# Kernel optimization log

Measured on AMD Instinct MI355X. Metric: run time of the kernel, lower is better.

## Reference

```python
import math
import jax, jax.numpy as jnp
import numpy as np

NUM_LAYERS = 2
D = 128
H = 8
CTX = 16
B, M, T = 4, 16, 256


def _lin(x, W, b):
    # torch nn.Linear: y = x @ W^T + b, W: [out, in]
    return jnp.einsum('...d,ed->...e', x, W) + b


def _ln(x, g, b, eps=1e-6):
    mu = jnp.mean(x, axis=-1, keepdims=True)
    v = jnp.mean((x - mu) ** 2, axis=-1, keepdims=True)
    return (x - mu) / jnp.sqrt(v + eps) * g + b


def _context_attention(x, L):
    # Faithful vectorization of the per-position python loop in ContextAttention.
    # Zero left-padding is NOT masked in the softmax (pad keys give score 0),
    # exactly as in the torch original.
    b, m, t, d = x.shape
    xp = jnp.pad(x, ((0, 0), (0, 0), (L - 1, 0), (0, 0)))  # [b,m,t+L-1,d]
    idx = jnp.arange(t)[:, None] + jnp.arange(L)[None, :]   # [t,L] window indices
    win = xp[:, :, idx, :]                                  # [b,m,t,L,d]
    scores = jnp.einsum('bmtd,bmtld->bmtl', x, win) / math.sqrt(d)
    w = jax.nn.softmax(scores, axis=-1)
    return jnp.einsum('bmtl,bmtld->bmtd', w, win)


def setup_inputs():
    key = jax.random.key(0)
    ks = jax.random.split(key, 8)
    L = NUM_LAYERS

    def w(k, shape):
        return jax.random.normal(k, shape, dtype=jnp.float32) * 0.02

    return {
        'x': jax.random.normal(ks[0], (B, M, T, D), dtype=jnp.float32),
        'Wq': w(ks[1], (L, D, D)), 'bq': jnp.zeros((L, D), jnp.float32),
        'Wk': w(ks[2], (L, D, D)), 'bk': jnp.zeros((L, D), jnp.float32),
        'Wv': w(ks[3], (L, D, D)), 'bv': jnp.zeros((L, D), jnp.float32),
        'Wo': w(ks[4], (L, D, D)), 'bo': jnp.zeros((L, D), jnp.float32),
        'W1': w(ks[5], (L, 4 * D, D)), 'b1': jnp.zeros((L, 4 * D), jnp.float32),
        'W2': w(ks[6], (L, D, 4 * D)), 'b2': jnp.zeros((L, D), jnp.float32),
        'ln1_g': jnp.ones((L, D), jnp.float32), 'ln1_b': jnp.zeros((L, D), jnp.float32),
        'ln2_g': jnp.ones((L, D), jnp.float32), 'ln2_b': jnp.zeros((L, D), jnp.float32),
        'lnf_g': jnp.ones((D,), jnp.float32), 'lnf_b': jnp.zeros((D,), jnp.float32),
        'context_len': CTX,
    }


def reference(x, Wq, bq, Wk, bk, Wv, bv, Wo, bo, W1, b1, W2, b2,
              ln1_g, ln1_b, ln2_g, ln2_b, lnf_g, lnf_b, context_len):
    b, m, t, d = x.shape
    dk = d // H

    def mha(xin, i):
        q = _lin(xin, Wq[i], bq[i])
        k = _lin(xin, Wk[i], bk[i])
        v = _lin(xin, Wv[i], bv[i])
        cq = _context_attention(q, context_len).reshape(b, m, t, H, dk)
        ck = _context_attention(k, context_len).reshape(b, m, t, H, dk)
        vr = v.reshape(b, m, t, H, dk)
        # full attention over time axis
        s = jnp.einsum('bmqhd,bmkhd->bmhqk', cq, ck) / math.sqrt(dk)
        xa = jnp.einsum('bmhqk,bmkhd->bmqhd', jax.nn.softmax(s, axis=-1), vr)
        # relational attention over the asset axis m
        s2 = jnp.einsum('bqthd,bkthd->bthqk', xa, xa) / math.sqrt(dk)
        xr = jnp.einsum('bthqk,bkthd->bthqd', jax.nn.softmax(s2, axis=-1), xa)
        # torch: permute((3,0,1,2,4)) -> [m,b,t,h,dk], then .view(b,m,t,d)
        xr = jnp.transpose(xr, (3, 0, 1, 2, 4)).reshape(b, m, t, d)
        return _lin(xr, Wo[i], bo[i])

    def ffn(xin, i):
        return _lin(jax.nn.relu(_lin(xin, W1[i], b1[i])), W2[i], b2[i])

    y = x
    for i in range(Wq.shape[0]):
        y = y + mha(_ln(y, ln1_g[i], ln1_b[i]), i)
        y = y + ffn(_ln(y, ln2_g[i], ln2_b[i]), i)
    return _ln(y, lnf_g, lnf_b)
```

## Files before the change

### kernel.cpp

```cpp
#include <hip/hip_runtime.h>
#include <cstddef>
#include <cstdint>

static constexpr int D_ = 128;
static constexpr int NROW = 16384;
static constexpr size_t S_ = (size_t)NROW * D_;

typedef __attribute__((ext_vector_type(8))) short bf16x8;
typedef __attribute__((ext_vector_type(4))) float f32x4;
typedef __attribute__((ext_vector_type(16))) float f32x16;
typedef __attribute__((ext_vector_type(8))) unsigned short ushortx8;

__device__ __forceinline__ unsigned short f2bf(float f) {
  unsigned int u = __float_as_uint(f);
  u += 0x7fff + ((u >> 16) & 1);
  return (unsigned short)(u >> 16);
}
__device__ __forceinline__ float bf2f(unsigned short h) {
  return __uint_as_float(((unsigned int)h) << 16);
}
__device__ __forceinline__ unsigned int cvt_pk_bf16(float lo, float hi) {
  unsigned int r;
  asm volatile("v_cvt_pk_bf16_f32 %0, %1, %2" : "=v"(r) : "v"(lo), "v"(hi));
  return r;
}
__device__ __forceinline__ float wsum64(float s) {
#pragma unroll
  for (int off = 32; off >= 1; off >>= 1) s += __shfl_xor(s, off);
  return s;
}

__global__ __launch_bounds__(256) void prep_kernel(
    const float* __restrict__ X,
    const float* __restrict__ Wq, const float* __restrict__ Wk,
    const float* __restrict__ Wv, const float* __restrict__ Wo,
    const float* __restrict__ W1, const float* __restrict__ W2,
    const float* __restrict__ bq, const float* __restrict__ bk,
    const float* __restrict__ bv, const float* __restrict__ bo,
    const float* __restrict__ b1, const float* __restrict__ b2,
    const float* __restrict__ g, const float* __restrict__ b,
    unsigned short* __restrict__ Wb, float* __restrict__ Bs,
    unsigned short* __restrict__ Ab) {
  int bx = blockIdx.x;
  if (bx < 192) {
    size_t i = ((size_t)bx * 256 + threadIdx.x) * 8;
    int layer = i >= 196608;
    size_t o = i - (size_t)layer * 196608;
    const float* src; size_t off;
    if      (o < 16384)  { src = Wq + layer * 16384; off = o; }
    else if (o < 32768)  { src = Wk + layer * 16384; off = o - 16384; }
    else if (o < 49152)  { src = Wv + layer * 16384; off = o - 32768; }
    else if (o < 65536)  { src = Wo + layer * 16384; off = o - 49152; }
    else if (o < 131072) { src = W1 + layer * 65536; off = o - 65536; }
    else                 { src = W2 + layer * 65536; off = o - 131072; }
    ushortx8 r;
#pragma unroll
    for (int j = 0; j < 8; j++) r[j] = f2bf(src[off + j]);
    *(ushortx8*)(Wb + i) = r;
  } else if (bx < 201) {
    int tid = (bx - 192) * 256 + threadIdx.x;
    if (tid >= 2304) return;
    int layer = tid / 1152, o = tid % 1152;
    float v;
    if      (o < 128)  v = bq[layer * 128 + o];
    else if (o < 256)  v = bk[layer * 128 + o - 128];
    else if (o < 384)  v = bv[layer * 128 + o - 256];
    else if (o < 512)  v = bo[layer * 128 + o - 384];
    else if (o < 1024) v = b1[layer * 512 + o - 512];
    else               v = b2[layer * 128 + o - 1024];
    Bs[tid] = v;
  } else {
    int wid = threadIdx.x >> 6, lane = threadIdx.x & 63;
    int row = ((bx - 201) << 2) + wid;
    float2 xv = *(const float2*)(X + (size_t)row * D_ + lane * 2);
    float s = wsum64(xv.x + xv.y);
    float sq = wsum64(xv.x * xv.x + xv.y * xv.y);
    float mu = s * (1.0f / 128.0f);
    float var = sq * (1.0f / 128.0f) - mu * mu;
    float rstd = rsqrtf(var + 1e-6f);
    float2 gv = *(const float2*)(g + lane * 2);
    float2 bv2 = *(const float2*)(b + lane * 2);
    unsigned int lo = f2bf((xv.x - mu) * rstd * gv.x + bv2.x);
    unsigned int hi = f2bf((xv.y - mu) * rstd * gv.y + bv2.y);
    *(unsigned int*)(Ab + (size_t)row * D_ + lane * 2) = lo | (hi << 16);
  }
}

template <int NT, int ROWW>
__global__ __launch_bounds__(512, 2) void gemm_kernel(
    const unsigned short* __restrict__ A, int lda,
    const unsigned short* __restrict__ W, int ldw,
    const float* __restrict__ bias,
    unsigned short* __restrict__ Cb, int K) {
  constexpr int COLW = 8 / ROWW;
  const int w = threadIdx.x >> 6;
  const int l = threadIdx.x & 63;
  const int rw = w / COLW, cw = w % COLW;
  const int r0 = blockIdx.x * (16 * ROWW) + rw * 16;
  const int c0 = cw * (NT * 16);
  const int lr = l & 15, lk = (l >> 4) * 8;
  f32x4 acc[NT] = {};
  const unsigned short* Ap = A + (size_t)(r0 + lr) * lda + lk;
  const unsigned short* Wp = W + (size_t)(c0 + lr) * ldw + lk;
  for (int kb = 0; kb < K; kb += 128) {
    bf16x8 aF[4];
    bf16x8 wF[4][NT];
#pragma unroll
    for (int kt = 0; kt < 4; ++kt) {
      int k0 = kb + kt * 32;
      aF[kt] = *(const bf16x8*)(Ap + k0);
#pragma unroll
      for (int n = 0; n < NT; ++n)
        wF[kt][n] = *(const bf16x8*)(Wp + (size_t)(n * 16) * ldw + k0);
    }
#pragma unroll
    for (int kt = 0; kt < 4; ++kt)
#pragma unroll
      for (int n = 0; n < NT; ++n)
        acc[n] = __builtin_amdgcn_mfma_f32_16x16x32_bf16(aF[kt], wF[kt][n], acc[n], 0, 0, 0);
  }
  const int rb = (l >> 4) * 4;
#pragma unroll
  for (int n = 0; n < NT; ++n) {
    int col = c0 + n * 16 + lr;
    float bval = bias[col];
    unsigned short* dst = Cb + (size_t)(col >> 7) * S_ + (col & 127);
#pragma unroll
    for (int j = 0; j < 4; ++j)
      dst[(size_t)(r0 + rb + j) * 128] = f2bf(acc[n][j] + bval);
  }
}

static constexpr int LDH = 136;
__global__ __launch_bounds__(512, 2) void ffn_kernel(
    const unsigned short* __restrict__ Abuf,
    const unsigned short* __restrict__ Wo_, const unsigned short* __restrict__ W1_,
    const unsigned short* __restrict__ W2_, const float* __restrict__ Bl,
    const float* __restrict__ rin,
    const float* __restrict__ ln2G, const float* __restrict__ ln2B,
    const float* __restrict__ lnxG, const float* __restrict__ lnxB,
    float* __restrict__ Yout, unsigned short* __restrict__ AbOut, int finalMode) {
  __shared__ unsigned short As[64][LDH];
  __shared__ unsigned short Hs[64][LDH];
  __shared__ unsigned short Mid[64][LDH];
  __shared__ float2 lnred[64][8];
  const int tid = threadIdx.x;
  const int w = tid >> 6, l = tid & 63;
  const int r0 = blockIdx.x * 64;
  const int lr = l & 15, lk = (l >> 4) * 8, rb = (l >> 4) * 4;
  const int col = w * 16 + lr;

  bf16x8 wof[4], w1f[4], w2f[4];
#pragma unroll
  for (int kt = 0; kt < 4; ++kt) {
    wof[kt] = *(const bf16x8*)(Wo_ + (size_t)col * 128 + kt * 32 + lk);
    w1f[kt] = *(const bf16x8*)(W1_ + (size_t)col * 128 + kt * 32 + lk);
    w2f[kt] = *(const bf16x8*)(W2_ + (size_t)col * 512 + kt * 32 + lk);
  }
#pragma unroll
  for (int itr = 0; itr < 2; ++itr) {
    int idx = itr * 512 + tid;
    int r = idx >> 4, c8 = (idx & 15) * 8;
    *(ushortx8*)&As[r][c8] = *(const ushortx8*)(Abuf + (size_t)(r0 + r) * 128 + c8);
  }
  __syncthreads();

  f32x4 acc1[4] = {};
#pragma unroll
  for (int kt = 0; kt < 4; ++kt)
#pragma unroll
    for (int m = 0; m < 4; ++m) {
      bf16x8 a = *(const bf16x8*)&As[m * 16 + lr][kt * 32 + lk];
      acc1[m] = __builtin_amdgcn_mfma_f32_16x16x32_bf16(a, wof[kt], acc1[m], 0, 0, 0);
    }
  float yreg[4][4];
  {
    float bval = Bl[384 + col];
#pragma unroll
    for (int m = 0; m < 4; ++m)
#pragma unroll
      for (int j = 0; j < 4; ++j)
        yreg[m][j] = acc1[m][j] + bval + rin[(size_t)(r0 + m * 16 + rb + j) * 128 + col];
  }
  {
    float s[4][4], sq[4][4];
#pragma unroll
    for (int m = 0; m < 4; ++m)
#pragma unroll
      for (int j = 0; j < 4; ++j) { s[m][j] = yreg[m][j]; sq[m][j] = yreg[m][j] * yreg[m][j]; }
#pragma unroll
    for (int off = 1; off < 16; off <<= 1)
#pragma unroll
      for (int m = 0; m < 4; ++m)
#pragma unroll
        for (int j = 0; j < 4; ++j) {
          s[m][j] += __shfl_xor(s[m][j], off);
          sq[m][j] += __shfl_xor(sq[m][j], off);
        }
    if (lr == 0)
#pragma unroll
      for (int m = 0; m < 4; ++m)
#pragma unroll
        for (int j = 0; j < 4; ++j)
          lnred[m * 16 + rb + j][w] = make_float2(s[m][j], sq[m][j]);
    __syncthreads();
    if (tid < 64) {
      float ts = 0.f, tq = 0.f;
#pragma unroll
      for (int k = 0; k < 8; ++k) { float2 p = lnred[tid][k]; ts += p.x; tq += p.y; }
      float mu = ts * (1.0f / 128.0f);
      float rstd = rsqrtf(tq * (1.0f / 128.0f) - mu * mu + 1e-6f);
      lnred[tid][0] = make_float2(mu, rstd);
    }
    __syncthreads();
    float g = ln2G[col], bb = ln2B[col];
#pragma unroll
    for (int m = 0; m < 4; ++m)
#pragma unroll
      for (int j = 0; j < 4; ++j) {
        float2 st = lnred[m * 16 + rb + j][0];
        Hs[m * 16 + rb + j][col] = f2bf((yreg[m][j] - st.x) * st.y * g + bb);
      }
  }
  __syncthreads();
  f32x4 acc2[4] = {};
#pragma unroll
  for (int c = 0; c < 4; ++c) {
    bf16x8 w1n[4], w2n[4];
    if (c < 3) {
#pragma unroll
      for (int kt = 0; kt < 4; ++kt) {
        w1n[kt] = *(const bf16x8*)(W1_ + (size_t)((c + 1) * 128 + col) * 128 + kt * 32 + lk);
        w2n[kt] = *(const bf16x8*)(W2_ + (size_t)col * 512 + (c + 1) * 128 + kt * 32 + lk);
      }
    }
    f32x4 accm[4] = {};
#pragma unroll
    for (int kt = 0; kt < 4; ++kt)
#pragma unroll
      for (int m = 0; m < 4; ++m) {
        bf16x8 a = *(const bf16x8*)&Hs[m * 16 + lr][kt * 32 + lk];
        accm[m] = __builtin_amdgcn_mfma_f32_16x16x32_bf16(a, w1f[kt], accm[m], 0, 0, 0);
      }
    float b1v = Bl[512 + c * 128 + col];
#pragma unroll
    for (int m = 0; m < 4; ++m)
#pragma unroll
      for (int j = 0; j < 4; ++j)
        Mid[m * 16 + rb + j][col] = f2bf(fmaxf(accm[m][j] + b1v, 0.f));
    __syncthreads();
#pragma unroll
    for (int kt = 0; kt < 4; ++kt)
#pragma unroll
      for (int m = 0; m < 4; ++m) {
        bf16x8 a = *(const bf16x8*)&Mid[m * 16 + lr][kt * 32 + lk];
        acc2[m] = __builtin_amdgcn_mfma_f32_16x16x32_bf16(a, w2f[kt], acc2[m], 0, 0, 0);
      }
    __syncthreads();
    if (c < 3) {
#pragma unroll
      for (int kt = 0; kt < 4; ++kt) { w1f[kt] = w1n[kt]; w2f[kt] = w2n[kt]; }
    }
  }
  float vfin[4][4];
  {
    float bval = Bl[1024 + col];
    float s[4][4], sq[4][4];
#pragma unroll
    for (int m = 0; m < 4; ++m)
#pragma unroll
      for (int j = 0; j < 4; ++j) {
        float v = acc2[m][j] + bval + yreg[m][j];
        vfin[m][j] = v;
        s[m][j] = v;
        sq[m][j] = v * v;
      }
#pragma unroll
    for (int off = 1; off < 16; off <<= 1)
#pragma unroll
      for (int m = 0; m < 4; ++m)
#pragma unroll
        for (int j = 0; j < 4; ++j) {
          s[m][j] += __shfl_xor(s[m][j], off);
          sq[m][j] += __shfl_xor(sq[m][j], off);
        }
    if (lr == 0)
#pragma unroll
      for (int m = 0; m < 4; ++m)
#pragma unroll
        for (int j = 0; j < 4; ++j)
          lnred[m * 16 + rb + j][w] = make_float2(s[m][j], sq[m][j]);
    __syncthreads();
    if (tid < 64) {
      float ts = 0.f, tq = 0.f;
#pragma unroll
      for (int k = 0; k < 8; ++k) { float2 p = lnred[tid][k]; ts += p.x; tq += p.y; }
      float mu = ts * (1.0f / 128.0f);
      float rstd = rsqrtf(tq * (1.0f / 128.0f) - mu * mu + 1e-6f);
      lnred[tid][0] = make_float2(mu, rstd);
    }
    __syncthreads();
    float g = lnxG[col], bb = lnxB[col];
#pragma unroll
    for (int m = 0; m < 4; ++m)
#pragma unroll
      for (int j = 0; j < 4; ++j) {
        int row = r0 + m * 16 + rb + j;
        float2 st = lnred[m * 16 + rb + j][0];
        float t = (vfin[m][j] - st.x) * st.y * g + bb;
        if (finalMode == 0) {
          Yout[(size_t)row * 128 + col] = vfin[m][j];
          AbOut[(size_t)row * 128 + col] = f2bf(t);
        } else {
          Yout[(size_t)row * 128 + col] = t;
        }
      }
  }
}

static constexpr int CTXLD = 134;
__global__ __launch_bounds__(128) void ctx_kernel(
    const unsigned short* __restrict__ qin, const unsigned short* __restrict__ kin,
    unsigned short* __restrict__ cqo, unsigned short* __restrict__ cko) {
  __shared__ float xs[47 * CTXLD];
  const unsigned short* src = blockIdx.y ? kin : qin;
  unsigned short* dst = blockIdx.y ? cko : cqo;
  const size_t rbase = (size_t)blockIdx.x * 256;
  const int t0 = blockIdx.z * 32;
  const int tid = threadIdx.x;
#pragma unroll
  for (int it = 0; it < 6; ++it) {
    int idx = it * 128 + tid;
    int i = idx >> 4, c8 = (idx & 15) * 8;
    if (i < 47) {
      int rg = t0 - 15 + i;
      float f[8];
      if (rg >= 0) {
        ushortx8 wv = *(const ushortx8*)(src + (rbase + rg) * 128 + c8);
#pragma unroll
        for (int j = 0; j < 8; ++j) f[j] = bf2f(wv[j]);
      } else {
#pragma unroll
        for (int j = 0; j < 8; ++j) f[j] = 0.f;
      }
      int base = i * CTXLD + c8 + (c8 >> 5) * 2;
#pragma unroll
      for (int j = 0; j < 8; j += 2)
        *(float2*)&xs[base + j] = make_float2(f[j], f[j + 1]);
    }
  }
  __syncthreads();
  const int ql = tid >> 2, qu = tid & 3;
  const int cb = qu * 34;
  const int cg = qu * 32;
  float ow[32];
#pragma unroll
  for (int c = 0; c < 32; c += 2) {
    float2 w = *(const float2*)&xs[(ql + 15) * CTXLD + cb + c];
    ow[c] = w.x; ow[c + 1] = w.y;
  }
  float p[16];
#pragma unroll
  for (int l = 0; l < 16; ++l) {
    const float* row = &xs[(ql + l) * CTXLD + cb];
    float d = 0.f;
#pragma unroll
    for (int c = 0; c < 32; c += 2) {
      float2 w = *(const float2*)(row + c);
      d = fmaf(ow[c], w.x, d);
      d = fmaf(ow[c + 1], w.y, d);
    }
    p[l] = d;
  }
  float den = 0.f;
#pragma unroll
  for (int l = 0; l < 16; ++l) {
    float sc = p[l] + __shfl_xor(p[l], 1);
    sc += __shfl_xor(sc, 2);
    p[l] = __expf(sc * 0.08838834764831845f);
    den += p[l];
  }
  float o[32];
#pragma unroll
  for (int c = 0; c < 32; ++c) o[c] = 0.f;
#pragma unroll
  for (int l = 0; l < 16; ++l) {
    float pl = p[l];
    const float* row = &xs[(ql + l) * CTXLD + cb];
#pragma unroll
    for (int c = 0; c < 32; c += 2) {
      float2 w = *(const float2*)(row + c);
      o[c] = fmaf(pl, w.x, o[c]);
      o[c + 1] = fmaf(pl, w.y, o[c + 1]);
    }
  }
  float inv = 1.0f / den;
  unsigned short* op = dst + (rbase + t0 + ql) * 128 + cg;
#pragma unroll
  for (int c8 = 0; c8 < 4; ++c8) {
    ushortx8 r;
#pragma unroll
    for (int j = 0; j < 8; ++j) r[j] = f2bf(o[c8 * 8 + j] * inv);
    *(ushortx8*)(op + c8 * 8) = r;
  }
}

static constexpr int PW = 272;
__global__ __launch_bounds__(256) void attn1_kernel(
    const unsigned short* __restrict__ cq, const unsigned short* __restrict__ ck,
    unsigned short* __restrict__ v) {
  __shared__ unsigned short vt[16][PW];
  __shared__ unsigned short ps[4][32][PW];
  __shared__ float rsum[4][32];
  const int bm = blockIdx.x >> 3, h = blockIdx.x & 7;
  const size_t rbase = (size_t)bm * 256;
  const int cbase = h * 16;
  const int tid = threadIdx.x;
  {
    ushortx8 v0 = *(const ushortx8*)(v + (rbase + tid) * 128 + cbase);
    ushortx8 v1 = *(const ushortx8*)(v + (rbase + tid) * 128 + cbase + 8);
#pragma unroll
    for (int d = 0; d < 8; ++d) { vt[d][tid] = v0[d]; vt[8 + d][tid] = v1[d]; }
  }
  __syncthreads();
  const int wid = tid >> 6, lane = tid & 63;
  const int l31 = lane & 31, l15 = lane & 15;
  const int hi5 = lane >> 5, hi4 = lane >> 4;
#pragma unroll
  for (int qt = 0; qt < 2; ++qt) {
    const int q0 = (wid * 2 + qt) * 32;
    bf16x8 bq = *(const bf16x8*)(cq + (rbase + q0 + l31) * 128 + cbase + hi5 * 8);
    float lsum = 0.f;
#pragma unroll
    for (int kt = 0; kt < 8; ++kt) {
      bf16x8 ak = *(const bf16x8*)(ck + (rbase + kt * 32 + l31) * 128 + cbase + hi5 * 8);
      f32x16 z = {};
      f32x16 s = __builtin_amdgcn_mfma_f32_32x32x16_bf16(ak, bq, z, 0, 0, 0);
      float p[16];
#pragma unroll
      for (int r = 0; r < 16; ++r) { p[r] = __expf(s[r] * 0.25f); lsum += p[r]; }
#pragma unroll
      for (int r = 0; r < 16; r += 2) {
        unsigned int pk = cvt_pk_bf16(p[r], p[r + 1]);
        int key = kt * 32 + (r & 3) + 8 * (r >> 2) + 4 * hi5;
        *(unsigned int*)&ps[wid][l31][key] = pk;
      }
    }
    lsum += __shfl_xor(lsum, 32);
    if (lane < 32) rsum[wid][lane] = 1.0f / lsum;
#pragma unroll
    for (int m = 0; m < 2; ++m) {
      f32x4 o = {};
#pragma unroll
      for (int k2 = 0; k2 < 8; ++k2) {
        bf16x8 pa = *(const bf16x8*)&ps[wid][m * 16 + l15][k2 * 32 + hi4 * 8];
        bf16x8 vb = *(const bf16x8*)&vt[l15][k2 * 32 + hi4 * 8];
        o = __builtin_amdgcn_mfma_f32_16x16x32_bf16(pa, vb, o, 0, 0, 0);
      }
      unsigned short* dst = v + (rbase + q0 + m * 16 + hi4 * 4) * 128 + cbase + l15;
#pragma unroll
      for (int j = 0; j < 4; ++j) {
        float inv = rsum[wid][m * 16 + hi4 * 4 + j];
        dst[(size_t)j * 128] = f2bf(o[j] * inv);
      }
    }
  }
}

__global__ __launch_bounds__(128) void attn2_kernel(
    const unsigned short* __restrict__ xa, unsigned short* __restrict__ xr) {
  __shared__ float xas[16][128];
  int b = blockIdx.x >> 8, t = blockIdx.x & 255;
  int tid = threadIdx.x;
#pragma unroll
  for (int jj = 0; jj < 2; ++jj) {
    int idx = tid + (jj << 7);
    int r = idx >> 4, c8 = (idx & 15) * 8;
    ushortx8 vv = *(const ushortx8*)(xa + ((size_t)((b * 16 + r) * 256 + t)) * 128 + c8);
#pragma unroll
    for (int j = 0; j < 8; ++j) xas[r][c8 + j] = bf2f(vv[j]);
  }
  __syncthreads();
  int h = tid >> 4, q = tid & 15;
  float xq[16];
#pragma unroll
  for (int d = 0; d < 16; d++) xq[d] = xas[q][h * 16 + d];
  float sc[16];
  float mx = -1e30f;
#pragma unroll
  for (int k = 0; k < 16; k++) {
    float s = 0.f;
#pragma unroll
    for (int d = 0; d < 16; d++) s += xq[d] * xas[k][h * 16 + d];
    s *= 0.25f;
    sc[k] = s;
    mx = fmaxf(mx, s);
  }
  float den = 0.f;
#pragma unroll
  for (int k = 0; k < 16; k++) { sc[k] = __expf(sc[k] - mx); den += sc[k]; }
  float inv = 1.0f / den;
  float out[16] = {};
#pragma unroll
  for (int k = 0; k < 16; k++) {
    float w = sc[k];
#pragma unroll
    for (int d = 0; d < 16; d++) out[d] += w * xas[k][h * 16 + d];
  }
  int g = q * 4 + b;
  unsigned short* dstp = xr + ((size_t)(g * 256 + t)) * 128 + h * 16;
  ushortx8 r0;
#pragma unroll
  for (int j = 0; j < 8; ++j) r0[j] = f2bf(out[j] * inv);
  *(ushortx8*)dstp = r0;
#pragma unroll
  for (int j = 0; j < 8; ++j) r0[j] = f2bf(out[8 + j] * inv);
  *(ushortx8*)(dstp + 8) = r0;
}

extern "C" void kernel_launch(void* const* d_in, const int* in_sizes, int n_in,
                              void* d_out, int out_size, void* d_ws, size_t ws_size,
                              hipStream_t stream) {
  const float* x    = (const float*)d_in[0];
  const float* Wq   = (const float*)d_in[1];
  const float* bq   = (const float*)d_in[2];
  const float* Wk   = (const float*)d_in[3];
  const float* bk   = (const float*)d_in[4];
  const float* Wv   = (const float*)d_in[5];
  const float* bv   = (const float*)d_in[6];
  const float* Wo   = (const float*)d_in[7];
  const float* bo   = (const float*)d_in[8];
  const float* W1   = (const float*)d_in[9];
  const float* b1   = (const float*)d_in[10];
  const float* W2   = (const float*)d_in[11];
  const float* b2   = (const float*)d_in[12];
  const float* ln1g = (const float*)d_in[13];
  const float* ln1b = (const float*)d_in[14];
  const float* ln2g = (const float*)d_in[15];
  const float* ln2b = (const float*)d_in[16];
  const float* lnfg = (const float*)d_in[17];
  const float* lnfb = (const float*)d_in[18];

  char* base = (char*)d_ws;
  unsigned short* CQb = (unsigned short*)base;
  unsigned short* CKb = (unsigned short*)(base + (4u  << 20));
  unsigned short* Qb  = (unsigned short*)(base + (8u  << 20));
  unsigned short* Kb  = (unsigned short*)(base + (12u << 20));
  unsigned short* Vb  = (unsigned short*)(base + (16u << 20));
  unsigned short* Ab  = (unsigned short*)(base + (20u << 20));
  unsigned short* Wb  = (unsigned short*)(base + (24u << 20));
  float*          Bs  = (float*)(base + (24u << 20) + 786432);
  float*          Y   = (float*)d_out;

  prep_kernel<<<4297, 256, 0, stream>>>(x, Wq, Wk, Wv, Wo, W1, W2,
                                        bq, bk, bv, bo, b1, b2,
                                        ln1g, ln1b, Wb, Bs, Ab);

  for (int i = 0; i < 2; ++i) {
    const float* rin = i ? Y : x;
    const unsigned short* Wl = Wb + (size_t)i * 196608;
    const float* Bl = Bs + i * 1152;
    gemm_kernel<3, 1><<<1024, 512, 0, stream>>>(Ab, 128, Wl, 128, Bl, Qb, 128);
    ctx_kernel<<<dim3(64, 2, 8), 128, 0, stream>>>(Qb, Kb, CQb, CKb);
    attn1_kernel<<<512, 256, 0, stream>>>(CQb, CKb, Vb);
    attn2_kernel<<<1024, 128, 0, stream>>>(Vb, Ab);
    if (i == 0) {
      ffn_kernel<<<256, 512, 0, stream>>>(Ab, Wl + 49152, Wl + 65536, Wl + 131072, Bl,
          rin, ln2g, ln2b, ln1g + 128, ln1b + 128, Y, Ab, 0);
    } else {
      ffn_kernel<<<256, 512, 0, stream>>>(Ab, Wl + 49152, Wl + 65536, Wl + 131072, Bl,
          rin, ln2g + 128, ln2b + 128, lnfg, lnfb, Y, nullptr, 1);
    }
  }
}
```

Measured before the change: 186.9 us.

## Retile FFN kernel to 32-row blocks with 4 waves covering 32 columns each

The fused Wo+LN+FFN kernel now processes 32 rows per block with 256 threads, and each wave computes two 16-column tiles instead of one. This doubles the grid from 256 to 512 blocks, which fills more of the CUs, and lets each A-fragment read from shared memory feed two MFMAs. It also removes one barrier per layernorm by having every lane reduce the per-row statistics itself, and it loads the residual input early. In exchange, each wave holds more registers for weight fragments, and weights are re-read by twice as many blocks.

```diff
diff --git a/kernel.cpp b/kernel.cpp
--- a/kernel.cpp
+++ b/kernel.cpp
@@ -132,7 +132,7 @@
 }
 
 static constexpr int LDH = 136;
-__global__ __launch_bounds__(512, 2) void ffn_kernel(
+__global__ __launch_bounds__(256, 2) void ffn_kernel(
     const unsigned short* __restrict__ Abuf,
     const unsigned short* __restrict__ Wo_, const unsigned short* __restrict__ W1_,
     const unsigned short* __restrict__ W2_, const float* __restrict__ Bl,
@@ -140,58 +140,77 @@
     const float* __restrict__ ln2G, const float* __restrict__ ln2B,
     const float* __restrict__ lnxG, const float* __restrict__ lnxB,
     float* __restrict__ Yout, unsigned short* __restrict__ AbOut, int finalMode) {
-  __shared__ unsigned short As[64][LDH];
-  __shared__ unsigned short Hs[64][LDH];
-  __shared__ unsigned short Mid[64][LDH];
-  __shared__ float2 lnred[64][8];
+  __shared__ unsigned short As[32][LDH];
+  __shared__ unsigned short Hs[32][LDH];
+  __shared__ unsigned short Mid[32][LDH];
+  __shared__ float2 lnred[32][4];
   const int tid = threadIdx.x;
   const int w = tid >> 6, l = tid & 63;
-  const int r0 = blockIdx.x * 64;
+  const int r0 = blockIdx.x * 32;
   const int lr = l & 15, lk = (l >> 4) * 8, rb = (l >> 4) * 4;
-  const int col = w * 16 + lr;
-
-  bf16x8 wof[4], w1f[4], w2f[4];
-#pragma unroll
-  for (int kt = 0; kt < 4; ++kt) {
-    wof[kt] = *(const bf16x8*)(Wo_ + (size_t)col * 128 + kt * 32 + lk);
-    w1f[kt] = *(const bf16x8*)(W1_ + (size_t)col * 128 + kt * 32 + lk);
-    w2f[kt] = *(const bf16x8*)(W2_ + (size_t)col * 512 + kt * 32 + lk);
+  const int cbase = w * 32;
+
+  float rv[2][2][4];
+#pragma unroll
+  for (int m = 0; m < 2; ++m)
+#pragma unroll
+    for (int n = 0; n < 2; ++n) {
+      int col = cbase + n * 16 + lr;
+#pragma unroll
+      for (int j = 0; j < 4; ++j)
+        rv[m][n][j] = rin[(size_t)(r0 + m * 16 + rb + j) * 128 + col];
+    }
+  bf16x8 wof[4][2], w1f[4][2];
+#pragma unroll
+  for (int n = 0; n < 2; ++n) {
+    int col = cbase + n * 16 + lr;
+#pragma unroll
+    for (int kt = 0; kt < 4; ++kt) {
+      wof[kt][n] = *(const bf16x8*)(Wo_ + (size_t)col * 128 + kt * 32 + lk);
+      w1f[kt][n] = *(const bf16x8*)(W1_ + (size_t)col * 128 + kt * 32 + lk);
+    }
   }
 #pragma unroll
   for (int itr = 0; itr < 2; ++itr) {
-    int idx = itr * 512 + tid;
+    int idx = itr * 256 + tid;
     int r = idx >> 4, c8 = (idx & 15) * 8;
     *(ushortx8*)&As[r][c8] = *(const ushortx8*)(Abuf + (size_t)(r0 + r) * 128 + c8);
   }
   __syncthreads();
 
-  f32x4 acc1[4] = {};
+  f32x4 acc1[2][2] = {};
 #pragma unroll
   for (int kt = 0; kt < 4; ++kt)
 #pragma unroll
-    for (int m = 0; m < 4; ++m) {
+    for (int m = 0; m < 2; ++m) {
       bf16x8 a = *(const bf16x8*)&As[m * 16 + lr][kt * 32 + lk];
-      acc1[m] = __builtin_amdgcn_mfma_f32_16x16x32_bf16(a, wof[kt], acc1[m], 0, 0, 0);
-    }
-  float yreg[4][4];
+#pragma unroll
+      for (int n = 0; n < 2; ++n)
+        acc1[m][n] = __builtin_amdgcn_mfma_f32_16x16x32_bf16(a, wof[kt][n], acc1[m][n], 0, 0, 0);
+    }
+  float yreg[2][2][4];
+#pragma unroll
+  for (int n = 0; n < 2; ++n) {
+    float bval = Bl[384 + cbase + n * 16 + lr];
+#pragma unroll
+    for (int m = 0; m < 2; ++m)
+#pragma unroll
+      for (int j = 0; j < 4; ++j)
+        yreg[m][n][j] = acc1[m][n][j] + bval + rv[m][n][j];
+  }
   {
-    float bval = Bl[384 + col];
-#pragma unroll
-    for (int m = 0; m < 4; ++m)
-#pragma unroll
-      for (int j = 0; j < 4; ++j)
-        yreg[m][j] = acc1[m][j] + bval + rin[(size_t)(r0 + m * 16 + rb + j) * 128 + col];
-  }
-  {
-    float s[4][4], sq[4][4];
-#pragma unroll
-    for (int m = 0; m < 4; ++m)
-#pragma unroll
-      for (int j = 0; j < 4; ++j) { s[m][j] = yreg[m][j]; sq[m][j] = yreg[m][j] * yreg[m][j]; }
+    float s[2][4], sq[2][4];
+#pragma unroll
+    for (int m = 0; m < 2; ++m)
+#pragma unroll
+      for (int j = 0; j < 4; ++j) {
+        s[m][j] = yreg[m][0][j] + yreg[m][1][j];
+        sq[m][j] = yreg[m][0][j] * yreg[m][0][j] + yreg[m][1][j] * yreg[m][1][j];
+      }
 #pragma unroll
     for (int off = 1; off < 16; off <<= 1)
 #pragma unroll
-      for (int m = 0; m < 4; ++m)
+      for (int m = 0; m < 2; ++m)
 #pragma unroll
         for (int j = 0; j < 4; ++j) {
           s[m][j] += __shfl_xor(s[m][j], off);
@@ -199,86 +218,105 @@
         }
     if (lr == 0)
 #pragma unroll
-      for (int m = 0; m < 4; ++m)
+      for (int m = 0; m < 2; ++m)
 #pragma unroll
         for (int j = 0; j < 4; ++j)
           lnred[m * 16 + rb + j][w] = make_float2(s[m][j], sq[m][j]);
     __syncthreads();
-    if (tid < 64) {
-      float ts = 0.f, tq = 0.f;
-#pragma unroll
-      for (int k = 0; k < 8; ++k) { float2 p = lnred[tid][k]; ts += p.x; tq += p.y; }
-      float mu = ts * (1.0f / 128.0f);
-      float rstd = rsqrtf(tq * (1.0f / 128.0f) - mu * mu + 1e-6f);
-      lnred[tid][0] = make_float2(mu, rstd);
+#pragma unroll
+    for (int m = 0; m < 2; ++m)
+#pragma unroll
+      for (int j = 0; j < 4; ++j) {
+        int row = m * 16 + rb + j;
+        float ts = 0.f, tq = 0.f;
+#pragma unroll
+        for (int k = 0; k < 4; ++k) { float2 p = lnred[row][k]; ts += p.x; tq += p.y; }
+        float mu = ts * (1.0f / 128.0f);
+        float rstd = rsqrtf(tq * (1.0f / 128.0f) - mu * mu + 1e-6f);
+#pragma unroll
+        for (int n = 0; n < 2; ++n) {
+          int col = cbase + n * 16 + lr;
+          Hs[row][col] = f2bf((yreg[m][n][j] - mu) * rstd * ln2G[col] + ln2B[col]);
+        }
+      }
+  }
+  __syncthreads();
+  f32x4 acc2[2][2] = {};
+#pragma unroll
+  for (int c = 0; c < 4; ++c) {
+    bf16x8 w2f[4][2], w1n[4][2];
+#pragma unroll
+    for (int n = 0; n < 2; ++n) {
+      int col = cbase + n * 16 + lr;
+#pragma unroll
+      for (int kt = 0; kt < 4; ++kt) {
+        w2f[kt][n] = *(const bf16x8*)(W2_ + (size_t)col * 512 + c * 128 + kt * 32 + lk);
+        if (c < 3)
+          w1n[kt][n] = *(const bf16x8*)(W1_ + (size_t)((c + 1) * 128 + col) * 128 + kt * 32 + lk);
+      }
+    }
+    f32x4 accm[2][2] = {};
+#pragma unroll
+    for (int kt = 0; kt < 4; ++kt)
+#pragma unroll
+      for (int m = 0; m < 2; ++m) {
+        bf16x8 a = *(const bf16x8*)&Hs[m * 16 + lr][kt * 32 + lk];
+#pragma unroll
+        for (int n = 0; n < 2; ++n)
+          accm[m][n] = __builtin_amdgcn_mfma_f32_16x16x32_bf16(a, w1f[kt][n], accm[m][n], 0, 0, 0);
+      }
+#pragma unroll
+    for (int n = 0; n < 2; ++n) {
+      float b1v = Bl[512 + c * 128 + cbase + n * 16 + lr];
+      int col = cbase + n * 16 + lr;
+#pragma unroll
+      for (int m = 0; m < 2; ++m)
+#pragma unroll
+        for (int j = 0; j < 4; ++j)
+          Mid[m * 16 + rb + j][col] = f2bf(fmaxf(accm[m][n][j] + b1v, 0.f));
     }
     __syncthreads();
-    float g = ln2G[col], bb = ln2B[col];
-#pragma unroll
-    for (int m = 0; m < 4; ++m)
-#pragma unroll
-      for (int j = 0; j < 4; ++j) {
-        float2 st = lnred[m * 16 + rb + j][0];
-        Hs[m * 16 + rb + j][col] = f2bf((yreg[m][j] - st.x) * st.y * g + bb);
-      }
-  }
-  __syncthreads();
-  f32x4 acc2[4] = {};
-#pragma unroll
-  for (int c = 0; c < 4; ++c) {
-    bf16x8 w1n[4], w2n[4];
-    if (c < 3) {
-#pragma unroll
-      for (int kt = 0; kt < 4; ++kt) {
-        w1n[kt] = *(const bf16x8*)(W1_ + (size_t)((c + 1) * 128 + col) * 128 + kt * 32 + lk);
-        w2n[kt] = *(const bf16x8*)(W2_ + (size_t)col * 512 + (c + 1) * 128 + kt * 32 + lk);
-      }
-    }
-    f32x4 accm[4] = {};
 #pragma unroll
     for (int kt = 0; kt < 4; ++kt)
 #pragma unroll
-      for (int m = 0; m < 4; ++m) {
-        bf16x8 a = *(const bf16x8*)&Hs[m * 16 + lr][kt * 32 + lk];
-        accm[m] = __builtin_amdgcn_mfma_f32_16x16x32_bf16(a, w1f[kt], accm[m], 0, 0, 0);
-      }
-    float b1v = Bl[512 + c * 128 + col];
-#pragma unroll
-    for (int m = 0; m < 4; ++m)
-#pragma unroll
-      for (int j = 0; j < 4; ++j)
-        Mid[m * 16 + rb + j][col] = f2bf(fmaxf(accm[m][j] + b1v, 0.f));
-    __syncthreads();
-#pragma unroll
-    for (int kt = 0; kt < 4; ++kt)
-#pragma unroll
-      for (int m = 0; m < 4; ++m) {
+      for (int m = 0; m < 2; ++m) {
         bf16x8 a = *(const bf16x8*)&Mid[m * 16 + lr][kt * 32 + lk];
-        acc2[m] = __builtin_amdgcn_mfma_f32_16x16x32_bf16(a, w2f[kt], acc2[m], 0, 0, 0);
+#pragma unroll
+        for (int n = 0; n < 2; ++n)
+          acc2[m][n] = __builtin_amdgcn_mfma_f32_16x16x32_bf16(a, w2f[kt][n], acc2[m][n], 0, 0, 0);
       }
     __syncthreads();
     if (c < 3) {
 #pragma unroll
-      for (int kt = 0; kt < 4; ++kt) { w1f[kt] = w1n[kt]; w2f[kt] = w2n[kt]; }
-    }
-  }
-  float vfin[4][4];
+      for (int kt = 0; kt < 4; ++kt)
+#pragma unroll
+        for (int n = 0; n < 2; ++n) w1f[kt][n] = w1n[kt][n];
+    }
+  }
   {
-    float bval = Bl[1024 + col];
-    float s[4][4], sq[4][4];
-#pragma unroll
-    for (int m = 0; m < 4; ++m)
-#pragma unroll
-      for (int j = 0; j < 4; ++j) {
-        float v = acc2[m][j] + bval + yreg[m][j];
-        vfin[m][j] = v;
-        s[m][j] = v;
-        sq[m][j] = v * v;
-      }
+    float vfin[2][2][4];
+    float s[2][4], sq[2][4];
+#pragma unroll
+    for (int m = 0; m < 2; ++m)
+#pragma unroll
+      for (int j = 0; j < 4; ++j) { s[m][j] = 0.f; sq[m][j] = 0.f; }
+#pragma unroll
+    for (int n = 0; n < 2; ++n) {
+      float bval = Bl[1024 + cbase + n * 16 + lr];
+#pragma unroll
+      for (int m = 0; m < 2; ++m)
+#pragma unroll
+        for (int j = 0; j < 4; ++j) {
+          float v = acc2[m][n][j] + bval + yreg[m][n][j];
+          vfin[m][n][j] = v;
+          s[m][j] += v;
+          sq[m][j] = fmaf(v, v, sq[m][j]);
+        }
+    }
 #pragma unroll
     for (int off = 1; off < 16; off <<= 1)
 #pragma unroll
-      for (int m = 0; m < 4; ++m)
+      for (int m = 0; m < 2; ++m)
 #pragma unroll
         for (int j = 0; j < 4; ++j) {
           s[m][j] += __shfl_xor(s[m][j], off);
@@ -286,33 +324,32 @@
         }
     if (lr == 0)
 #pragma unroll
-      for (int m = 0; m < 4; ++m)
+      for (int m = 0; m < 2; ++m)
 #pragma unroll
         for (int j = 0; j < 4; ++j)
           lnred[m * 16 + rb + j][w] = make_float2(s[m][j], sq[m][j]);
     __syncthreads();
-    if (tid < 64) {
-      float ts = 0.f, tq = 0.f;
-#pragma unroll
-      for (int k = 0; k < 8; ++k) { float2 p = lnred[tid][k]; ts += p.x; tq += p.y; }
-      float mu = ts * (1.0f / 128.0f);
-      float rstd = rsqrtf(tq * (1.0f / 128.0f) - mu * mu + 1e-6f);
-      lnred[tid][0] = make_float2(mu, rstd);
-    }
-    __syncthreads();
-    float g = lnxG[col], bb = lnxB[col];
-#pragma unroll
-    for (int m = 0; m < 4; ++m)
+#pragma unroll
+    for (int m = 0; m < 2; ++m)
 #pragma unroll
       for (int j = 0; j < 4; ++j) {
-        int row = r0 + m * 16 + rb + j;
-        float2 st = lnred[m * 16 + rb + j][0];
-        float t = (vfin[m][j] - st.x) * st.y * g + bb;
-        if (finalMode == 0) {
-          Yout[(size_t)row * 128 + col] = vfin[m][j];
-          AbOut[(size_t)row * 128 + col] = f2bf(t);
-        } else {
-          Yout[(size_t)row * 128 + col] = t;
+        int row = m * 16 + rb + j;
+        float ts = 0.f, tq = 0.f;
+#pragma unroll
+        for (int k = 0; k < 4; ++k) { float2 p = lnred[row][k]; ts += p.x; tq += p.y; }
+        float mu = ts * (1.0f / 128.0f);
+        float rstd = rsqrtf(tq * (1.0f / 128.0f) - mu * mu + 1e-6f);
+#pragma unroll
+        for (int n = 0; n < 2; ++n) {
+          int col = cbase + n * 16 + lr;
+          int grow = r0 + row;
+          float t = (vfin[m][n][j] - mu) * rstd * lnxG[col] + lnxB[col];
+          if (finalMode == 0) {
+            Yout[(size_t)grow * 128 + col] = vfin[m][n][j];
+            AbOut[(size_t)grow * 128 + col] = f2bf(t);
+          } else {
+            Yout[(size_t)grow * 128 + col] = t;
+          }
         }
       }
   }
@@ -565,10 +602,10 @@
     attn1_kernel<<<512, 256, 0, stream>>>(CQb, CKb, Vb);
     attn2_kernel<<<1024, 128, 0, stream>>>(Vb, Ab);
     if (i == 0) {
-      ffn_kernel<<<256, 512, 0, stream>>>(Ab, Wl + 49152, Wl + 65536, Wl + 131072, Bl,
+      ffn_kernel<<<512, 256, 0, stream>>>(Ab, Wl + 49152, Wl + 65536, Wl + 131072, Bl,
           rin, ln2g, ln2b, ln1g + 128, ln1b + 128, Y, Ab, 0);
     } else {
-      ffn_kernel<<<256, 512, 0, stream>>>(Ab, Wl + 49152, Wl + 65536, Wl + 131072, Bl,
+      ffn_kernel<<<512, 256, 0, stream>>>(Ab, Wl + 49152, Wl + 65536, Wl + 131072, Bl,
           rin, ln2g + 128, ln2b + 128, lnfg, lnfb, Y, nullptr, 1);
     }
   }
```

New measurement: 192.6 us. 3.0% more time.
